# Kernel tuning notes

Measured on AMD Instinct MI355X. Metric: run time of the kernel, lower is better.

The kernel has to match this reference:

```python
import jax, jax.numpy as jnp
import numpy as np

B = 262144
I = 128  # input_size
H = 128  # hidden_size


def setup_inputs() -> dict:
    key = jax.random.key(0)
    ks = jax.random.split(key, 12)
    std = 1.0 / np.sqrt(H)
    u = lambda k, shape: jax.random.uniform(k, shape, jnp.float32, -std, std)
    return {
        "inputs": jax.random.normal(ks[0], (B, I), jnp.float32),
        "h_prev": jax.random.normal(ks[1], (B, H), jnp.float32),
        "c_prev": jax.random.normal(ks[2], (B, H), jnp.float32),
        "W_ii": u(ks[3], (H, I)), "W_hi": u(ks[4], (H, H)),
        "W_if": u(ks[5], (H, I)), "W_hf": u(ks[6], (H, H)),
        "W_io": u(ks[7], (H, I)), "W_ho": u(ks[8], (H, H)),
        "W_ig": u(ks[9], (H, I)), "W_hg": u(ks[10], (H, H)),
    }


def reference(inputs, h_prev, c_prev, W_ii, W_hi, W_if, W_hf, W_io, W_ho, W_ig, W_hg):
    # Same math as 8 separate GEMMs, expressed as 2 fused GEMMs over concatenated gates.
    W_x = jnp.concatenate([W_ii, W_if, W_io, W_ig], axis=0)  # [4H, I]
    W_h = jnp.concatenate([W_hi, W_hf, W_ho, W_hg], axis=0)  # [4H, H]
    gates = inputs @ W_x.T + h_prev @ W_h.T  # [B, 4H]
    gi, gf, go, gg = jnp.split(gates, 4, axis=-1)
    i_t = jax.nn.sigmoid(gi)
    f_t = jax.nn.sigmoid(gf)
    o_t = jax.nn.sigmoid(go)
    g_t = jnp.tanh(gg)
    c_t = f_t * c_prev + i_t * g_t
    h_t = o_t * jnp.tanh(c_t)
    return jnp.stack([h_t, c_t], axis=0)  # [2, B, H]
```

## Files before the change

### kernel.cpp

```cpp
#include <hip/hip_runtime.h>

#define BATCH 262144
#define TILES (BATCH / 64)
#define ASTRIDE 280
#define BH 33554432

typedef __attribute__((ext_vector_type(8))) short bf16x8;
typedef __attribute__((ext_vector_type(4))) float f32x4;

__device__ __forceinline__ unsigned short f2bf(float f) {
  unsigned int u = __float_as_uint(f);
  u += 0x7fffu + ((u >> 16) & 1u);
  return (unsigned short)(u >> 16);
}

__device__ __forceinline__ float fexp(float x) { return __builtin_amdgcn_exp2f(x * 1.44269504f); }
__device__ __forceinline__ float sigm(float x) { return __builtin_amdgcn_rcpf(1.f + fexp(-x)); }
__device__ __forceinline__ float ftanh(float x) { return 1.f - 2.f * __builtin_amdgcn_rcpf(1.f + fexp(2.f * x)); }

__global__ __launch_bounds__(512, 2) void lstm_fused(
    const float* __restrict__ X, const float* __restrict__ H0, const float* __restrict__ C0,
    const float* __restrict__ Wii, const float* __restrict__ Whi,
    const float* __restrict__ Wif, const float* __restrict__ Whf,
    const float* __restrict__ Wio, const float* __restrict__ Who,
    const float* __restrict__ Wig, const float* __restrict__ Whg,
    float* __restrict__ Out) {
  __shared__ unsigned short Abuf[64 * ASTRIDE];

  const int tid = threadIdx.x;
  const int wave = tid >> 6;
  const int lane = tid & 63;
  const int lrow = lane & 15;
  const int lk = (lane >> 4) * 8;
  const int hcol = wave * 16 + lrow;

  const float* Wxp[4] = {Wii, Wif, Wio, Wig};
  const float* Whp[4] = {Whi, Whf, Who, Whg};

  bf16x8 wf[4][8];
#pragma unroll
  for (int g = 0; g < 4; ++g) {
#pragma unroll
    for (int kk = 0; kk < 8; ++kk) {
      const int k = kk * 32 + lk;
      const float* src = (kk < 4) ? (Wxp[g] + hcol * 128 + k)
                                  : (Whp[g] + hcol * 128 + (k - 128));
      float4 lo = *(const float4*)src;
      float4 hi = *(const float4*)(src + 4);
      bf16x8 w;
      w[0] = (short)f2bf(lo.x); w[1] = (short)f2bf(lo.y);
      w[2] = (short)f2bf(lo.z); w[3] = (short)f2bf(lo.w);
      w[4] = (short)f2bf(hi.x); w[5] = (short)f2bf(hi.y);
      w[6] = (short)f2bf(hi.z); w[7] = (short)f2bf(hi.w);
      wf[g][kk] = w;
    }
  }

  for (int tile = blockIdx.x; tile < TILES; tile += gridDim.x) {
    const int row0 = tile * 64;

    const float4* xin = (const float4*)(X + (size_t)row0 * 128);
    const float4* hin = (const float4*)(H0 + (size_t)row0 * 128);
#pragma unroll
    for (int j = 0; j < 4; ++j) {
      const int f = tid + j * 512;
      const int r = f >> 5;
      const int c4 = (f & 31) * 4;
      float4 v = xin[f];
      ushort4 p;
      p.x = f2bf(v.x); p.y = f2bf(v.y); p.z = f2bf(v.z); p.w = f2bf(v.w);
      *(ushort4*)&Abuf[r * ASTRIDE + c4] = p;
      float4 u = hin[f];
      ushort4 q;
      q.x = f2bf(u.x); q.y = f2bf(u.y); q.z = f2bf(u.z); q.w = f2bf(u.w);
      *(ushort4*)&Abuf[r * ASTRIDE + 128 + c4] = q;
    }
    __syncthreads();

#pragma unroll
    for (int mt = 0; mt < 4; ++mt) {
      f32x4 acc0 = {0.f, 0.f, 0.f, 0.f};
      f32x4 acc1 = acc0, acc2 = acc0, acc3 = acc0;
#pragma unroll
      for (int kk = 0; kk < 8; ++kk) {
        bf16x8 a = *(const bf16x8*)&Abuf[(mt * 16 + lrow) * ASTRIDE + kk * 32 + lk];
        acc0 = __builtin_amdgcn_mfma_f32_16x16x32_bf16(a, wf[0][kk], acc0, 0, 0, 0);
        acc1 = __builtin_amdgcn_mfma_f32_16x16x32_bf16(a, wf[1][kk], acc1, 0, 0, 0);
        acc2 = __builtin_amdgcn_mfma_f32_16x16x32_bf16(a, wf[2][kk], acc2, 0, 0, 0);
        acc3 = __builtin_amdgcn_mfma_f32_16x16x32_bf16(a, wf[3][kk], acc3, 0, 0, 0);
      }
      const int rbase = row0 + mt * 16 + (lane >> 4) * 4;
#pragma unroll
      for (int j = 0; j < 4; ++j) {
        const int rg = rbase + j;
        const float cprev = C0[rg * 128 + hcol];
        const float it = sigm(acc0[j]);
        const float ft = sigm(acc1[j]);
        const float ot = sigm(acc2[j]);
        const float gt = ftanh(acc3[j]);
        const float ct = ft * cprev + it * gt;
        const float ht = ot * ftanh(ct);
        Out[rg * 128 + hcol] = ht;
        Out[BH + rg * 128 + hcol] = ct;
      }
    }
    __syncthreads();
  }
}

extern "C" void kernel_launch(void* const* d_in, const int* in_sizes, int n_in,
                              void* d_out, int out_size, void* d_ws, size_t ws_size,
                              hipStream_t stream) {
  (void)in_sizes; (void)n_in; (void)out_size; (void)d_ws; (void)ws_size;
  lstm_fused<<<256, 512, 0, stream>>>(
      (const float*)d_in[0], (const float*)d_in[1], (const float*)d_in[2],
      (const float*)d_in[3], (const float*)d_in[4], (const float*)d_in[5],
      (const float*)d_in[6], (const float*)d_in[7], (const float*)d_in[8],
      (const float*)d_in[9], (const float*)d_in[10],
      (float*)d_out);
}
```

Before: 190.9 us.

## Prefetch next tile's X/H into registers and batch C_prev loads before MFMA

Register-prefetches the next tile's input and hidden rows while the current tile computes, so global load latency overlaps the MFMA and gate math. All C_prev values for the tile are loaded up front instead of inside the epilogue. It also changes the per-thread load shape to 8-float chunks with 16-byte LDS stores, tightens the LDS row stride, and drops the trailing barrier. The cost is more VGPRs for the staged float4s and cv array, which at launch bounds 512x2 may cause spills. The iteration count is now hardcoded to the grid size.

```diff
diff --git a/kernel.cpp b/kernel.cpp
--- a/kernel.cpp
+++ b/kernel.cpp
@@ -1,12 +1,14 @@
 #include <hip/hip_runtime.h>
 
 #define BATCH 262144
-#define TILES (BATCH / 64)
-#define ASTRIDE 280
+#define NBLK 256
+#define NITER 16
+#define ASTRIDE 264
 #define BH 33554432
 
 typedef __attribute__((ext_vector_type(8))) short bf16x8;
 typedef __attribute__((ext_vector_type(4))) float f32x4;
+typedef __attribute__((ext_vector_type(8))) unsigned short u16x8;
 
 __device__ __forceinline__ unsigned short f2bf(float f) {
   unsigned int u = __float_as_uint(f);
@@ -25,7 +27,7 @@
     const float* __restrict__ Wio, const float* __restrict__ Who,
     const float* __restrict__ Wig, const float* __restrict__ Whg,
     float* __restrict__ Out) {
-  __shared__ unsigned short Abuf[64 * ASTRIDE];
+  __shared__ __align__(16) unsigned short Abuf[64 * ASTRIDE];
 
   const int tid = threadIdx.x;
   const int wave = tid >> 6;
@@ -56,26 +58,61 @@
     }
   }
 
-  for (int tile = blockIdx.x; tile < TILES; tile += gridDim.x) {
+  float4 sx[4], sh[4];
+
+  auto issue_loads = [&](int row0) {
+#pragma unroll
+    for (int j = 0; j < 2; ++j) {
+      const int f = tid + j * 512;
+      const int r = f >> 4;
+      const int c = (f & 15) * 8;
+      const float* px = X + (size_t)(row0 + r) * 128 + c;
+      sx[j * 2 + 0] = *(const float4*)px;
+      sx[j * 2 + 1] = *(const float4*)(px + 4);
+      const float* ph = H0 + (size_t)(row0 + r) * 128 + c;
+      sh[j * 2 + 0] = *(const float4*)ph;
+      sh[j * 2 + 1] = *(const float4*)(ph + 4);
+    }
+  };
+
+  issue_loads(blockIdx.x * 64);
+
+  for (int it = 0; it < NITER; ++it) {
+    const int tile = blockIdx.x + it * NBLK;
     const int row0 = tile * 64;
 
-    const float4* xin = (const float4*)(X + (size_t)row0 * 128);
-    const float4* hin = (const float4*)(H0 + (size_t)row0 * 128);
+    __syncthreads();
+
 #pragma unroll
-    for (int j = 0; j < 4; ++j) {
+    for (int j = 0; j < 2; ++j) {
       const int f = tid + j * 512;
-      const int r = f >> 5;
-      const int c4 = (f & 31) * 4;
-      float4 v = xin[f];
-      ushort4 p;
-      p.x = f2bf(v.x); p.y = f2bf(v.y); p.z = f2bf(v.z); p.w = f2bf(v.w);
-      *(ushort4*)&Abuf[r * ASTRIDE + c4] = p;
-      float4 u = hin[f];
-      ushort4 q;
-      q.x = f2bf(u.x); q.y = f2bf(u.y); q.z = f2bf(u.z); q.w = f2bf(u.w);
-      *(ushort4*)&Abuf[r * ASTRIDE + 128 + c4] = q;
+      const int r = f >> 4;
+      const int c = (f & 15) * 8;
+      u16x8 w;
+      w[0] = f2bf(sx[j * 2].x);     w[1] = f2bf(sx[j * 2].y);
+      w[2] = f2bf(sx[j * 2].z);     w[3] = f2bf(sx[j * 2].w);
+      w[4] = f2bf(sx[j * 2 + 1].x); w[5] = f2bf(sx[j * 2 + 1].y);
+      w[6] = f2bf(sx[j * 2 + 1].z); w[7] = f2bf(sx[j * 2 + 1].w);
+      *(u16x8*)&Abuf[r * ASTRIDE + c] = w;
+      u16x8 v;
+      v[0] = f2bf(sh[j * 2].x);     v[1] = f2bf(sh[j * 2].y);
+      v[2] = f2bf(sh[j * 2].z);     v[3] = f2bf(sh[j * 2].w);
+      v[4] = f2bf(sh[j * 2 + 1].x); v[5] = f2bf(sh[j * 2 + 1].y);
+      v[6] = f2bf(sh[j * 2 + 1].z); v[7] = f2bf(sh[j * 2 + 1].w);
+      *(u16x8*)&Abuf[r * ASTRIDE + 128 + c] = v;
     }
+
+    if (it + 1 < NITER) issue_loads(row0 + NBLK * 64);
+
     __syncthreads();
+
+    const int rb = row0 + (lane >> 4) * 4;
+    float cv[16];
+#pragma unroll
+    for (int mt = 0; mt < 4; ++mt)
+#pragma unroll
+      for (int j = 0; j < 4; ++j)
+        cv[mt * 4 + j] = C0[(size_t)(rb + mt * 16 + j) * 128 + hcol];
 
 #pragma unroll
     for (int mt = 0; mt < 4; ++mt) {
@@ -89,22 +126,21 @@
         acc2 = __builtin_amdgcn_mfma_f32_16x16x32_bf16(a, wf[2][kk], acc2, 0, 0, 0);
         acc3 = __builtin_amdgcn_mfma_f32_16x16x32_bf16(a, wf[3][kk], acc3, 0, 0, 0);
       }
-      const int rbase = row0 + mt * 16 + (lane >> 4) * 4;
+      const int rbase = rb + mt * 16;
 #pragma unroll
       for (int j = 0; j < 4; ++j) {
         const int rg = rbase + j;
-        const float cprev = C0[rg * 128 + hcol];
-        const float it = sigm(acc0[j]);
+        const float cprev = cv[mt * 4 + j];
+        const float it_ = sigm(acc0[j]);
         const float ft = sigm(acc1[j]);
         const float ot = sigm(acc2[j]);
         const float gt = ftanh(acc3[j]);
-        const float ct = ft * cprev + it * gt;
+        const float ct = ft * cprev + it_ * gt;
         const float ht = ot * ftanh(ct);
-        Out[rg * 128 + hcol] = ht;
-        Out[BH + rg * 128 + hcol] = ct;
+        Out[(size_t)rg * 128 + hcol] = ht;
+        Out[BH + (size_t)rg * 128 + hcol] = ct;
       }
     }
-    __syncthreads();
   }
 }
 
@@ -112,7 +148,7 @@
                               void* d_out, int out_size, void* d_ws, size_t ws_size,
                               hipStream_t stream) {
   (void)in_sizes; (void)n_in; (void)out_size; (void)d_ws; (void)ws_size;
-  lstm_fused<<<256, 512, 0, stream>>>(
+  lstm_fused<<<NBLK, 512, 0, stream>>>(
       (const float*)d_in[0], (const float*)d_in[1], (const float*)d_in[2],
       (const float*)d_in[3], (const float*)d_in[4], (const float*)d_in[5],
       (const float*)d_in[6], (const float*)d_in[7], (const float*)d_in[8],
```

Result: faster. 156.5 us (-18.0%).

## Software-pipeline tile loads with double-buffered LDS and register prefetch

Applied to the files above, without the earlier changes.

Restructures the persistent loop into a double-buffered pipeline. Loads of X, H0 and C0 for the next tile are issued into registers before the MFMA and epilogue of the current tile, and converted into an alternating LDS buffer. The grid grows to 512 blocks with a fixed 8 iterations each, and the LDS row stride and load pattern change to 8-wide vector stores. This hides global load latency behind compute, but raises register pressure under launch_bounds(512,2) and hardcodes the tile count.

```diff
diff --git a/kernel.cpp b/kernel.cpp
--- a/kernel.cpp
+++ b/kernel.cpp
@@ -1,12 +1,14 @@
 #include <hip/hip_runtime.h>
 
 #define BATCH 262144
-#define TILES (BATCH / 64)
-#define ASTRIDE 280
+#define NBLK 512
+#define NITER 8
+#define ASTRIDE 264
 #define BH 33554432
 
 typedef __attribute__((ext_vector_type(8))) short bf16x8;
 typedef __attribute__((ext_vector_type(4))) float f32x4;
+typedef __attribute__((ext_vector_type(8))) unsigned short u16x8;
 
 __device__ __forceinline__ unsigned short f2bf(float f) {
   unsigned int u = __float_as_uint(f);
@@ -25,7 +27,7 @@
     const float* __restrict__ Wio, const float* __restrict__ Who,
     const float* __restrict__ Wig, const float* __restrict__ Whg,
     float* __restrict__ Out) {
-  __shared__ unsigned short Abuf[64 * ASTRIDE];
+  __shared__ __align__(16) unsigned short Abuf[2][64 * ASTRIDE];
 
   const int tid = threadIdx.x;
   const int wave = tid >> 6;
@@ -33,6 +35,8 @@
   const int lrow = lane & 15;
   const int lk = (lane >> 4) * 8;
   const int hcol = wave * 16 + lrow;
+  const int r0 = tid >> 4;
+  const int cc = (tid & 15) * 8;
 
   const float* Wxp[4] = {Wii, Wif, Wio, Wig};
   const float* Whp[4] = {Whi, Whf, Who, Whg};
@@ -56,63 +60,98 @@
     }
   }
 
-  for (int tile = blockIdx.x; tile < TILES; tile += gridDim.x) {
-    const int row0 = tile * 64;
+  float4 sx0, sx1, sx2, sx3, sh0, sh1, sh2, sh3;
+  float cv0[16], cv1[16];
 
-    const float4* xin = (const float4*)(X + (size_t)row0 * 128);
-    const float4* hin = (const float4*)(H0 + (size_t)row0 * 128);
-#pragma unroll
-    for (int j = 0; j < 4; ++j) {
-      const int f = tid + j * 512;
-      const int r = f >> 5;
-      const int c4 = (f & 31) * 4;
-      float4 v = xin[f];
-      ushort4 p;
-      p.x = f2bf(v.x); p.y = f2bf(v.y); p.z = f2bf(v.z); p.w = f2bf(v.w);
-      *(ushort4*)&Abuf[r * ASTRIDE + c4] = p;
-      float4 u = hin[f];
-      ushort4 q;
-      q.x = f2bf(u.x); q.y = f2bf(u.y); q.z = f2bf(u.z); q.w = f2bf(u.w);
-      *(ushort4*)&Abuf[r * ASTRIDE + 128 + c4] = q;
-    }
-    __syncthreads();
+#define ISSUE_LOADS(ROW0) do {                                           \
+    const float* px_ = X + (size_t)((ROW0) + r0) * 128 + cc;             \
+    sx0 = *(const float4*)px_;  sx1 = *(const float4*)(px_ + 4);         \
+    const float* ph_ = H0 + (size_t)((ROW0) + r0) * 128 + cc;            \
+    sh0 = *(const float4*)ph_;  sh1 = *(const float4*)(ph_ + 4);         \
+    const float* qx_ = px_ + 32 * 128;                                   \
+    sx2 = *(const float4*)qx_;  sx3 = *(const float4*)(qx_ + 4);         \
+    const float* qh_ = ph_ + 32 * 128;                                   \
+    sh2 = *(const float4*)qh_;  sh3 = *(const float4*)(qh_ + 4);         \
+  } while (0)
 
-#pragma unroll
-    for (int mt = 0; mt < 4; ++mt) {
-      f32x4 acc0 = {0.f, 0.f, 0.f, 0.f};
-      f32x4 acc1 = acc0, acc2 = acc0, acc3 = acc0;
-#pragma unroll
-      for (int kk = 0; kk < 8; ++kk) {
-        bf16x8 a = *(const bf16x8*)&Abuf[(mt * 16 + lrow) * ASTRIDE + kk * 32 + lk];
-        acc0 = __builtin_amdgcn_mfma_f32_16x16x32_bf16(a, wf[0][kk], acc0, 0, 0, 0);
-        acc1 = __builtin_amdgcn_mfma_f32_16x16x32_bf16(a, wf[1][kk], acc1, 0, 0, 0);
-        acc2 = __builtin_amdgcn_mfma_f32_16x16x32_bf16(a, wf[2][kk], acc2, 0, 0, 0);
-        acc3 = __builtin_amdgcn_mfma_f32_16x16x32_bf16(a, wf[3][kk], acc3, 0, 0, 0);
-      }
-      const int rbase = row0 + mt * 16 + (lane >> 4) * 4;
-#pragma unroll
-      for (int j = 0; j < 4; ++j) {
-        const int rg = rbase + j;
-        const float cprev = C0[rg * 128 + hcol];
-        const float it = sigm(acc0[j]);
-        const float ft = sigm(acc1[j]);
-        const float ot = sigm(acc2[j]);
-        const float gt = ftanh(acc3[j]);
-        const float ct = ft * cprev + it * gt;
-        const float ht = ot * ftanh(ct);
-        Out[rg * 128 + hcol] = ht;
-        Out[BH + rg * 128 + hcol] = ct;
-      }
-    }
-    __syncthreads();
+#define ISSUE_CV(ROW0, CV) do {                                          \
+    const int rbv_ = (ROW0) + (lane >> 4) * 4;                           \
+    _Pragma("unroll")                                                    \
+    for (int mt_ = 0; mt_ < 4; ++mt_)                                    \
+      _Pragma("unroll")                                                  \
+      for (int j_ = 0; j_ < 4; ++j_)                                     \
+        CV[mt_ * 4 + j_] = C0[(size_t)(rbv_ + mt_ * 16 + j_) * 128 + hcol]; \
+  } while (0)
+
+#define CVT8(DST, A, B) do {                                             \
+    u16x8 t_;                                                            \
+    t_[0] = f2bf((A).x); t_[1] = f2bf((A).y);                            \
+    t_[2] = f2bf((A).z); t_[3] = f2bf((A).w);                            \
+    t_[4] = f2bf((B).x); t_[5] = f2bf((B).y);                            \
+    t_[6] = f2bf((B).z); t_[7] = f2bf((B).w);                            \
+    *(u16x8*)(DST) = t_;                                                 \
+  } while (0)
+
+#define BODY(IT, AB, CVR, CVW) do {                                      \
+    const int row0_ = (blockIdx.x + (IT) * NBLK) * 64;                   \
+                              \
+    CVT8(&(AB)[r0 * ASTRIDE + cc], sx0, sx1);                            \
+    CVT8(&(AB)[r0 * ASTRIDE + 128 + cc], sh0, sh1);                      \
+    CVT8(&(AB)[(r0 + 32) * ASTRIDE + cc], sx2, sx3);                     \
+    CVT8(&(AB)[(r0 + 32) * ASTRIDE + 128 + cc], sh2, sh3);               \
+    __syncthreads();        \
+      \
+                       \
+    if ((IT) + 1 < NITER) {                                              \
+      ISSUE_LOADS(row0_ + NBLK * 64);                                    \
+      ISSUE_CV(row0_ + NBLK * 64, CVW);                                  \
+    }                                                                    \
+    const int rb_ = row0_ + (lane >> 4) * 4;                             \
+    _Pragma("unroll")                                                    \
+    for (int mt = 0; mt < 4; ++mt) {                                     \
+      f32x4 a0 = {0.f, 0.f, 0.f, 0.f}, a1 = a0, a2 = a0, a3 = a0;        \
+      _Pragma("unroll")                                                  \
+      for (int kk = 0; kk < 8; ++kk) {                                   \
+        bf16x8 a = *(const bf16x8*)&(AB)[(mt * 16 + lrow) * ASTRIDE + kk * 32 + lk]; \
+        a0 = __builtin_amdgcn_mfma_f32_16x16x32_bf16(a, wf[0][kk], a0, 0, 0, 0); \
+        a1 = __builtin_amdgcn_mfma_f32_16x16x32_bf16(a, wf[1][kk], a1, 0, 0, 0); \
+        a2 = __builtin_amdgcn_mfma_f32_16x16x32_bf16(a, wf[2][kk], a2, 0, 0, 0); \
+        a3 = __builtin_amdgcn_mfma_f32_16x16x32_bf16(a, wf[3][kk], a3, 0, 0, 0); \
+      }                                                                  \
+      _Pragma("unroll")                                                  \
+      for (int j = 0; j < 4; ++j) {                                      \
+        const int rg = rb_ + mt * 16 + j;                                \
+        const float itv = sigm(a0[j]);                                   \
+        const float ftv = sigm(a1[j]);                                   \
+        const float otv = sigm(a2[j]);                                   \
+        const float gtv = ftanh(a3[j]);                                  \
+        const float ctv = ftv * (CVR)[mt * 4 + j] + itv * gtv;           \
+        const float htv = otv * ftanh(ctv);                              \
+        Out[(size_t)rg * 128 + hcol] = htv;                              \
+        Out[BH + (size_t)rg * 128 + hcol] = ctv;                         \
+      }                                                                  \
+    }                                                                    \
+  } while (0)
+
+  ISSUE_LOADS(blockIdx.x * 64);
+  ISSUE_CV(blockIdx.x * 64, cv0);
+
+  for (int it = 0; it < NITER; it += 2) {
+    BODY(it, &Abuf[0][0], cv0, cv1);
+    BODY(it + 1, &Abuf[1][0], cv1, cv0);
   }
+
+#undef ISSUE_LOADS
+#undef ISSUE_CV
+#undef CVT8
+#undef BODY
 }
 
 extern "C" void kernel_launch(void* const* d_in, const int* in_sizes, int n_in,
                               void* d_out, int out_size, void* d_ws, size_t ws_size,
                               hipStream_t stream) {
   (void)in_sizes; (void)n_in; (void)out_size; (void)d_ws; (void)ws_size;
-  lstm_fused<<<256, 512, 0, stream>>>(
+  lstm_fused<<<NBLK, 512, 0, stream>>>(
       (const float*)d_in[0], (const float*)d_in[1], (const float*)d_in[2],
       (const float*)d_in[3], (const float*)d_in[4], (const float*)d_in[5],
       (const float*)d_in[6], (const float*)d_in[7], (const float*)d_in[8],
```

Measured after the change: 180.6 us. 5.4% less time.
